# Kernel optimization log

Measured on AMD Instinct MI355X. Metric: run time of the kernel, lower is better.

## Reference

```python
import jax, jax.numpy as jnp
import numpy as np

T, H, W, C, HD, K = 4, 128, 128, 256, 8, 9
F = C // HD


def setup_inputs() -> dict:
    key = jax.random.key(0)
    ks = jax.random.split(key, 6)
    x = jax.random.normal(ks[0], (T, H, W, C), jnp.float32)
    attn = jax.random.uniform(ks[1], (1, HD, T, H, W, K), jnp.float32)
    attn = attn / attn.sum(-1, keepdims=True)  # softmax-normalized neighbor weights
    # integer flow offsets (dt, dh, dw) in [-3, 3], as produced by non-local search
    flows = jax.random.randint(ks[2], (1, HD, T, H, W, K, 3), -3, 4, jnp.int32)
    v_w = jax.random.normal(ks[3], (C, C), jnp.float32) * (C ** -0.5)
    proj_w = jax.random.normal(ks[4], (C, C), jnp.float32) * (C ** -0.5)
    proj_b = jnp.zeros((C,), jnp.float32)
    return dict(x=x, attn=attn, flows=flows, v_w=v_w, proj_w=proj_w, proj_b=proj_b)


def reference(x, attn, flows, v_w, proj_w, proj_b):
    T, H, W, C = x.shape
    HD = attn.shape[1]
    F = C // HD
    # v projection, split heads: [T,H,W,HD,F]
    v = (x @ v_w.T).reshape(T, H, W, HD, F)
    fl = flows[0]  # [HD,T,H,W,K,3] integer offsets (dt, dh, dw)
    tt = jnp.clip(jnp.arange(T)[None, :, None, None, None] + fl[..., 0], 0, T - 1)
    hh = jnp.clip(jnp.arange(H)[None, None, :, None, None] + fl[..., 1], 0, H - 1)
    ww = jnp.clip(jnp.arange(W)[None, None, None, :, None] + fl[..., 2], 0, W - 1)
    hd = jnp.arange(HD)[:, None, None, None, None]
    # flow-guided non-local gather: [HD,T,H,W,K,F]
    gathered = v[tt, hh, ww, hd]
    # attention-weighted sum over K neighbors, merge heads: [T,H,W,C]
    out = jnp.einsum('dthwk,dthwkf->thwdf', attn[0], gathered).reshape(T, H, W, C)
    # output projection
    return out @ proj_w.T + proj_b
```

## Files before the change

### kernel.cpp

```cpp
#include <hip/hip_runtime.h>
#include <hip/hip_bf16.h>

namespace {

constexpr int T = 4, H = 128, W = 128, C = 256, HD = 8, K = 9, F = 32;
constexpr int M = T * H * W;

typedef __attribute__((ext_vector_type(8))) short short8v;
typedef __attribute__((ext_vector_type(4))) float f32x4;

__device__ __forceinline__ unsigned short f2bf(float f) {
  unsigned u = __float_as_uint(f);
  unsigned r = (u + 0x7fffu + ((u >> 16) & 1u)) >> 16;
  return (unsigned short)r;
}

__device__ __forceinline__ float bf2f(unsigned short u) {
  return __uint_as_float(((unsigned)u) << 16);
}

template <int ALAYOUT, bool OUT_F32>
__global__ __launch_bounds__(256) void mfma_gemm(
    const void* __restrict__ Aptr, const float* __restrict__ Bw,
    void* __restrict__ Cptr, const float* __restrict__ bias) {
  __shared__ unsigned short As[128][40];
  __shared__ unsigned short Bs[128][40];
  const int m0 = blockIdx.x * 128;
  const int n0 = blockIdx.y * 128;
  const int t = threadIdx.x;
  const int lane = t & 63;
  const int wid = t >> 6;
  const int wm = wid >> 1, wn = wid & 1;
  const int fr = lane & 15;
  const int kg = lane >> 4;

  f32x4 acc[4][4];
#pragma unroll
  for (int ni = 0; ni < 4; ++ni) {
    float b = 0.f;
    if (OUT_F32) b = bias[n0 + wn * 64 + ni * 16 + fr];
#pragma unroll
    for (int mi = 0; mi < 4; ++mi) {
      acc[mi][ni][0] = b; acc[mi][ni][1] = b;
      acc[mi][ni][2] = b; acc[mi][ni][3] = b;
    }
  }

  for (int k0 = 0; k0 < C; k0 += 32) {
    __syncthreads();
    if (ALAYOUT == 2) {
      const unsigned short* Ab = (const unsigned short*)Aptr;
      const size_t hb = (size_t)(k0 >> 5) * M * 32;
#pragma unroll
      for (int i = 0; i < 2; ++i) {
        const int flat = t + i * 256;
        const int row = flat >> 2, kc = (flat & 3) * 8;
        *(short8v*)&As[row][kc] =
            *(const short8v*)(Ab + hb + (size_t)(m0 + row) * 32 + kc);
      }
    } else {
      const float* Af = (const float*)Aptr;
#pragma unroll
      for (int i = 0; i < 4; ++i) {
        const int flat = t + i * 256;
        const int row = flat >> 3, kc = (flat & 7) * 4;
        const float4 v4 = *(const float4*)(Af + (size_t)(m0 + row) * C + k0 + kc);
        ushort4 o;
        o.x = f2bf(v4.x); o.y = f2bf(v4.y); o.z = f2bf(v4.z); o.w = f2bf(v4.w);
        *(ushort4*)&As[row][kc] = o;
      }
    }
#pragma unroll
    for (int i = 0; i < 4; ++i) {
      const int flat = t + i * 256;
      const int row = flat >> 3, kc = (flat & 7) * 4;
      const float4 v4 = *(const float4*)(Bw + (size_t)(n0 + row) * C + k0 + kc);
      ushort4 o;
      o.x = f2bf(v4.x); o.y = f2bf(v4.y); o.z = f2bf(v4.z); o.w = f2bf(v4.w);
      *(ushort4*)&Bs[row][kc] = o;
    }
    __syncthreads();
    short8v af[4], bfv[4];
#pragma unroll
    for (int mi = 0; mi < 4; ++mi)
      af[mi] = *(const short8v*)&As[wm * 64 + mi * 16 + fr][kg * 8];
#pragma unroll
    for (int ni = 0; ni < 4; ++ni)
      bfv[ni] = *(const short8v*)&Bs[wn * 64 + ni * 16 + fr][kg * 8];
#pragma unroll
    for (int mi = 0; mi < 4; ++mi)
#pragma unroll
      for (int ni = 0; ni < 4; ++ni)
        acc[mi][ni] = __builtin_amdgcn_mfma_f32_16x16x32_bf16(
            af[mi], bfv[ni], acc[mi][ni], 0, 0, 0);
  }

#pragma unroll
  for (int mi = 0; mi < 4; ++mi) {
#pragma unroll
    for (int ni = 0; ni < 4; ++ni) {
      const int gcol = n0 + wn * 64 + ni * 16 + fr;
#pragma unroll
      for (int r = 0; r < 4; ++r) {
        const int grow = m0 + wm * 64 + mi * 16 + kg * 4 + r;
        if (OUT_F32) {
          ((float*)Cptr)[(size_t)grow * C + gcol] = acc[mi][ni][r];
        } else {
          ((unsigned short*)Cptr)[(size_t)grow * C + gcol] = f2bf(acc[mi][ni][r]);
        }
      }
    }
  }
}

struct __attribute__((packed, aligned(4))) I4p { int a, b, c, d; };
struct __attribute__((packed, aligned(4))) I2p { int a, b; };
struct __attribute__((packed, aligned(4))) F4p { float a, b, c, d; };

__global__ __launch_bounds__(256, 4) void gather_lds_kernel(
    const unsigned short* __restrict__ v, const float* __restrict__ attn,
    const int* __restrict__ flows, unsigned short* __restrict__ agg2) {
  __shared__ __align__(16) unsigned short halo[560 * 32];
  const int nb = (blockIdx.x & 7) * 512 + (blockIdx.x >> 3);
  const int head = nb & 7;
  const int tile = nb >> 3;
  const int h0 = (tile >> 5) * 8;
  const int w0 = (tile & 31) * 4;
  const int tid = threadIdx.x;
  const int o = tid >> 1;
  const int fh = tid & 1;
  const int tq = o >> 5;
  const int s = o & 31;
  const int h = h0 + (s >> 2);
  const int w = w0 + (s & 3);
  const int m = (tq << 14) | (h << 7) | w;
  const unsigned short* vhead = v + head * F;

  const int base = ((head << 16) | m) * K;
  const int fb = base * 3;
  const I4p f0 = *(const I4p*)(flows + fb + 0);
  const I4p f1 = *(const I4p*)(flows + fb + 4);
  const I4p f2 = *(const I4p*)(flows + fb + 8);
  const I4p f3 = *(const I4p*)(flows + fb + 12);
  const I4p f4 = *(const I4p*)(flows + fb + 16);
  const I4p f5 = *(const I4p*)(flows + fb + 20);
  const I2p f6 = *(const I2p*)(flows + fb + 24);
  const int f7 = flows[fb + 26];
  const F4p a0 = *(const F4p*)(attn + base + 0);
  const F4p a1 = *(const F4p*)(attn + base + 4);
  const float a2 = attn[base + 8];

  auto piece_src = [&](int pi, int& ldsoff) -> const short8v* {
    const int sliver = pi >> 2, j = pi & 3;
    const int tt = sliver / 140;
    const int rem = sliver - tt * 140;
    const int hh = rem / 10;
    const int ww = rem - hh * 10;
    const int hc = min(max(h0 - 3 + hh, 0), H - 1);
    const int wc = min(max(w0 - 3 + ww, 0), W - 1);
    const int sm = (tt << 14) | (hc << 7) | wc;
    const int jj = (j + (sliver >> 1)) & 3;
    ldsoff = sliver * 32 + jj * 8;
    return (const short8v*)(vhead + (size_t)sm * C + j * 8);
  };
  {
    short8v pc[8]; int lo[8];
#pragma unroll
    for (int e = 0; e < 8; ++e) pc[e] = *piece_src(tid + e * 256, lo[e]);
    short8v pt; int lot = 0;
    if (tid < 192) pt = *piece_src(2048 + tid, lot);
#pragma unroll
    for (int e = 0; e < 8; ++e) *(short8v*)&halo[lo[e]] = pc[e];
    if (tid < 192) *(short8v*)&halo[lot] = pt;
  }

  const int d[27] = {f0.a, f0.b, f0.c, f0.d, f1.a, f1.b, f1.c, f1.d,
                     f2.a, f2.b, f2.c, f2.d, f3.a, f3.b, f3.c, f3.d,
                     f4.a, f4.b, f4.c, f4.d, f5.a, f5.b, f5.c, f5.d,
                     f6.a, f6.b, f7};
  const float aw[9] = {a0.a, a0.b, a0.c, a0.d, a1.a, a1.b, a1.c, a1.d, a2};
  int row[9];
#pragma unroll
  for (int k = 0; k < 9; ++k) {
    const int ts = min(max(tq + d[3 * k + 0], 0), T - 1);
    const int hs = min(max(h + d[3 * k + 1], 0), H - 1) - (h0 - 3);
    const int ws = min(max(w + d[3 * k + 2], 0), W - 1) - (w0 - 3);
    row[k] = (ts * 14 + hs) * 10 + ws;
  }

  __syncthreads();

  float acc[16];
#pragma unroll
  for (int i = 0; i < 16; ++i) acc[i] = 0.f;
#pragma unroll
  for (int k = 0; k < 9; ++k) {
    const int rbase = row[k] * 32;
    const int rot = (row[k] >> 1) & 3;
#pragma unroll
    for (int jl = 0; jl < 2; ++jl) {
      const int j = fh * 2 + jl;
      const short8v p = *(const short8v*)&halo[rbase + (((j + rot) & 3)) * 8];
#pragma unroll
      for (int e = 0; e < 8; ++e)
        acc[jl * 8 + e] += aw[k] * bf2f((unsigned short)p[e]);
    }
  }

  unsigned short* dst = agg2 + ((size_t)head * M + m) * F + fh * 16;
#pragma unroll
  for (int jl = 0; jl < 2; ++jl) {
    short8v ov;
#pragma unroll
    for (int e = 0; e < 8; ++e) ov[e] = (short)f2bf(acc[jl * 8 + e]);
    *(short8v*)(dst + jl * 8) = ov;
  }
}

__global__ __launch_bounds__(256) void agg_proj_kernel(
    const unsigned short* __restrict__ v, const float* __restrict__ attn,
    const int* __restrict__ flows, const float* __restrict__ proj_w,
    const float* __restrict__ proj_b, float* __restrict__ out) {
  __shared__ float Agg[32][C];
  __shared__ float Bs[32][C];
  const int bid = blockIdx.x;
  const int t = bid >> 9;
  const int h0 = ((bid >> 5) & 15) * 8;
  const int w0 = (bid & 31) * 4;
  const int tid = threadIdx.x;

  const int g = tid >> 3;
  const int f4 = (tid & 7) * 4;
#pragma unroll
  for (int r = 0; r < 8; ++r) {
    const int pi = r * 32 + g;
    const int pos = pi >> 3;
    const int head = pi & 7;
    const int h = h0 + (pos >> 2);
    const int w = w0 + (pos & 3);
    const int base = (((head * T + t) * H + h) * W + w) * K;
    const int fbase = base * 3;
    float4 acc = {0.f, 0.f, 0.f, 0.f};
#pragma unroll
    for (int k = 0; k < K; ++k) {
      const int dt = flows[fbase + k * 3 + 0];
      const int dh = flows[fbase + k * 3 + 1];
      const int dw = flows[fbase + k * 3 + 2];
      const float aw = attn[base + k];
      const int tt = min(max(t + dt, 0), T - 1);
      const int hh = min(max(h + dh, 0), H - 1);
      const int ww = min(max(w + dw, 0), W - 1);
      const int mm = (tt * H + hh) * W + ww;
      const ushort4 r4 = *(const ushort4*)(v + (size_t)mm * C + head * F + f4);
      acc.x += aw * bf2f(r4.x);
      acc.y += aw * bf2f(r4.y);
      acc.z += aw * bf2f(r4.z);
      acc.w += aw * bf2f(r4.w);
    }
    *(float4*)&Agg[pos][head * F + f4] = acc;
  }
  __syncthreads();

  const int tx = tid & 31;
  const int ty = tid >> 5;
  float acc2[4][8];
  {
    const float4 b0 = *(const float4*)(proj_b + tx * 8);
    const float4 b1 = *(const float4*)(proj_b + tx * 8 + 4);
#pragma unroll
    for (int i = 0; i < 4; ++i) {
      acc2[i][0] = b0.x; acc2[i][1] = b0.y; acc2[i][2] = b0.z; acc2[i][3] = b0.w;
      acc2[i][4] = b1.x; acc2[i][5] = b1.y; acc2[i][6] = b1.z; acc2[i][7] = b1.w;
    }
  }
  for (int k0 = 0; k0 < C; k0 += 32) {
#pragma unroll
    for (int i = 0; i < 8; ++i) {
      const float4 w4 = *(const float4*)(proj_w + (size_t)tid * C + k0 + i * 4);
      Bs[i * 4 + 0][tid] = w4.x;
      Bs[i * 4 + 1][tid] = w4.y;
      Bs[i * 4 + 2][tid] = w4.z;
      Bs[i * 4 + 3][tid] = w4.w;
    }
    __syncthreads();
#pragma unroll 4
    for (int kk = 0; kk < 32; ++kk) {
      const float4 bb0 = *(const float4*)&Bs[kk][tx * 8];
      const float4 bb1 = *(const float4*)&Bs[kk][tx * 8 + 4];
      float a[4];
#pragma unroll
      for (int i = 0; i < 4; ++i) a[i] = Agg[ty * 4 + i][k0 + kk];
#pragma unroll
      for (int i = 0; i < 4; ++i) {
        acc2[i][0] += a[i] * bb0.x;
        acc2[i][1] += a[i] * bb0.y;
        acc2[i][2] += a[i] * bb0.z;
        acc2[i][3] += a[i] * bb0.w;
        acc2[i][4] += a[i] * bb1.x;
        acc2[i][5] += a[i] * bb1.y;
        acc2[i][6] += a[i] * bb1.z;
        acc2[i][7] += a[i] * bb1.w;
      }
    }
    __syncthreads();
  }
#pragma unroll
  for (int i = 0; i < 4; ++i) {
    const int pos = ty * 4 + i;
    const int h = h0 + (pos >> 2);
    const int w = w0 + (pos & 3);
    const int m = (t * H + h) * W + w;
    float4 o0, o1;
    o0.x = acc2[i][0]; o0.y = acc2[i][1]; o0.z = acc2[i][2]; o0.w = acc2[i][3];
    o1.x = acc2[i][4]; o1.y = acc2[i][5]; o1.z = acc2[i][6]; o1.w = acc2[i][7];
    *(float4*)(out + (size_t)m * C + tx * 8) = o0;
    *(float4*)(out + (size_t)m * C + tx * 8 + 4) = o1;
  }
}

}

extern "C" void kernel_launch(void* const* d_in, const int* in_sizes, int n_in,
                              void* d_out, int out_size, void* d_ws,
                              size_t ws_size, hipStream_t stream) {
  const float* x = (const float*)d_in[0];
  const float* attn = (const float*)d_in[1];
  const int* flows = (const int*)d_in[2];
  const float* v_w = (const float*)d_in[3];
  const float* proj_w = (const float*)d_in[4];
  const float* proj_b = (const float*)d_in[5];
  float* out = (float*)d_out;

  const size_t VBYTES = (size_t)M * C * 2;
  unsigned short* v = (unsigned short*)d_ws;

  dim3 g1(M / 128, C / 128);
  mfma_gemm<0, false><<<g1, 256, 0, stream>>>(x, v_w, v, nullptr);

  if (ws_size >= 2 * VBYTES) {
    unsigned short* agg2 = (unsigned short*)((char*)d_ws + VBYTES);
    gather_lds_kernel<<<4096, 256, 0, stream>>>(v, attn, flows, agg2);
    mfma_gemm<2, true><<<g1, 256, 0, stream>>>(agg2, proj_w, out, proj_b);
  } else {
    const int nblk = T * (H / 8) * (W / 4);
    agg_proj_kernel<<<nblk, 256, 0, stream>>>(v, attn, flows, proj_w, proj_b,
                                              out);
  }
}
```

Baseline: 97.66 us.

## Double-buffer LDS halo tiles and process four w-tiles per block

Each gather block now loops over four consecutive 4-wide w-tiles instead of one. The halo for the next tile and its flow/attn metadata are loaded into registers while the current tile is computed from a second LDS buffer. The goal is to overlap global-memory latency with the LDS gather-accumulate and to amortize block setup. In exchange the kernel needs twice the LDS and more registers, launch bounds drop to 2 blocks per CU, and the grid shrinks to 1024 blocks.

```diff
diff --git a/kernel.cpp b/kernel.cpp
--- a/kernel.cpp
+++ b/kernel.cpp
@@ -117,103 +117,146 @@
 struct __attribute__((packed, aligned(4))) I2p { int a, b; };
 struct __attribute__((packed, aligned(4))) F4p { float a, b, c, d; };
 
-__global__ __launch_bounds__(256, 4) void gather_lds_kernel(
+__global__ __launch_bounds__(256, 2) void gather_lds_kernel(
     const unsigned short* __restrict__ v, const float* __restrict__ attn,
     const int* __restrict__ flows, unsigned short* __restrict__ agg2) {
-  __shared__ __align__(16) unsigned short halo[560 * 32];
-  const int nb = (blockIdx.x & 7) * 512 + (blockIdx.x >> 3);
+  __shared__ __align__(16) unsigned short halo[2][560 * 32];
+  const int nb = (blockIdx.x & 7) * 128 + (blockIdx.x >> 3);
   const int head = nb & 7;
-  const int tile = nb >> 3;
-  const int h0 = (tile >> 5) * 8;
-  const int w0 = (tile & 31) * 4;
+  const int rest = nb >> 3;
+  const int h0 = (rest >> 3) * 8;
+  const int wgp = rest & 7;
+  const int w0base = wgp * 16;
   const int tid = threadIdx.x;
   const int o = tid >> 1;
   const int fh = tid & 1;
   const int tq = o >> 5;
   const int s = o & 31;
-  const int h = h0 + (s >> 2);
-  const int w = w0 + (s & 3);
-  const int m = (tq << 14) | (h << 7) | w;
+  const int hof = s >> 2, wof = s & 3;
+  const int h = h0 + hof;
   const unsigned short* vhead = v + head * F;
 
-  const int base = ((head << 16) | m) * K;
-  const int fb = base * 3;
-  const I4p f0 = *(const I4p*)(flows + fb + 0);
-  const I4p f1 = *(const I4p*)(flows + fb + 4);
-  const I4p f2 = *(const I4p*)(flows + fb + 8);
-  const I4p f3 = *(const I4p*)(flows + fb + 12);
-  const I4p f4 = *(const I4p*)(flows + fb + 16);
-  const I4p f5 = *(const I4p*)(flows + fb + 20);
-  const I2p f6 = *(const I2p*)(flows + fb + 24);
-  const int f7 = flows[fb + 26];
-  const F4p a0 = *(const F4p*)(attn + base + 0);
-  const F4p a1 = *(const F4p*)(attn + base + 4);
-  const float a2 = attn[base + 8];
-
-  auto piece_src = [&](int pi, int& ldsoff) -> const short8v* {
-    const int sliver = pi >> 2, j = pi & 3;
-    const int tt = sliver / 140;
-    const int rem = sliver - tt * 140;
-    const int hh = rem / 10;
-    const int ww = rem - hh * 10;
-    const int hc = min(max(h0 - 3 + hh, 0), H - 1);
-    const int wc = min(max(w0 - 3 + ww, 0), W - 1);
-    const int sm = (tt << 14) | (hc << 7) | wc;
-    const int jj = (j + (sliver >> 1)) & 3;
-    ldsoff = sliver * 32 + jj * 8;
-    return (const short8v*)(vhead + (size_t)sm * C + j * 8);
-  };
-  {
-    short8v pc[8]; int lo[8];
-#pragma unroll
-    for (int e = 0; e < 8; ++e) pc[e] = *piece_src(tid + e * 256, lo[e]);
-    short8v pt; int lot = 0;
-    if (tid < 192) pt = *piece_src(2048 + tid, lot);
-#pragma unroll
-    for (int e = 0; e < 8; ++e) *(short8v*)&halo[lo[e]] = pc[e];
-    if (tid < 192) *(short8v*)&halo[lot] = pt;
-  }
-
-  const int d[27] = {f0.a, f0.b, f0.c, f0.d, f1.a, f1.b, f1.c, f1.d,
-                     f2.a, f2.b, f2.c, f2.d, f3.a, f3.b, f3.c, f3.d,
-                     f4.a, f4.b, f4.c, f4.d, f5.a, f5.b, f5.c, f5.d,
-                     f6.a, f6.b, f7};
-  const float aw[9] = {a0.a, a0.b, a0.c, a0.d, a1.a, a1.b, a1.c, a1.d, a2};
-  int row[9];
-#pragma unroll
-  for (int k = 0; k < 9; ++k) {
-    const int ts = min(max(tq + d[3 * k + 0], 0), T - 1);
-    const int hs = min(max(h + d[3 * k + 1], 0), H - 1) - (h0 - 3);
-    const int ws = min(max(w + d[3 * k + 2], 0), W - 1) - (w0 - 3);
-    row[k] = (ts * 14 + hs) * 10 + ws;
-  }
-
+  short8v pc[8]; int lo[8]; short8v pt; int lot;
+  auto stage_load = [&](int w0t) {
+#pragma unroll
+    for (int e = 0; e < 8; ++e) {
+      const int pi = tid + e * 256;
+      const int sliver = pi >> 2, j = pi & 3;
+      const int tt = sliver / 140;
+      const int rem = sliver - tt * 140;
+      const int hh = rem / 10;
+      const int ww = rem - hh * 10;
+      const int hc = min(max(h0 - 3 + hh, 0), H - 1);
+      const int wc = min(max(w0t - 3 + ww, 0), W - 1);
+      const int sm = (tt << 14) | (hc << 7) | wc;
+      lo[e] = sliver * 32 + ((j + (sliver >> 1)) & 3) * 8;
+      pc[e] = *(const short8v*)(vhead + (size_t)sm * C + j * 8);
+    }
+    lot = -1;
+    if (tid < 192) {
+      const int pi = 2048 + tid;
+      const int sliver = pi >> 2, j = pi & 3;
+      const int tt = sliver / 140;
+      const int rem = sliver - tt * 140;
+      const int hh = rem / 10;
+      const int ww = rem - hh * 10;
+      const int hc = min(max(h0 - 3 + hh, 0), H - 1);
+      const int wc = min(max(w0t - 3 + ww, 0), W - 1);
+      const int sm = (tt << 14) | (hc << 7) | wc;
+      lot = sliver * 32 + ((j + (sliver >> 1)) & 3) * 8;
+      pt = *(const short8v*)(vhead + (size_t)sm * C + j * 8);
+    }
+  };
+  auto stage_write = [&](int buf) {
+    unsigned short* hb = halo[buf];
+#pragma unroll
+    for (int e = 0; e < 8; ++e) *(short8v*)&hb[lo[e]] = pc[e];
+    if (lot >= 0) *(short8v*)&hb[lot] = pt;
+  };
+
+  I4p f0, f1, f2, f3, f4, f5; I2p f6; int f7; F4p a0, a1; float a2;
+  auto meta_load = [&](int w0t) {
+    const int m_ = (tq << 14) | (h << 7) | (w0t + wof);
+    const int base = ((head << 16) | m_) * K;
+    const int fb = base * 3;
+    f0 = *(const I4p*)(flows + fb + 0);
+    f1 = *(const I4p*)(flows + fb + 4);
+    f2 = *(const I4p*)(flows + fb + 8);
+    f3 = *(const I4p*)(flows + fb + 12);
+    f4 = *(const I4p*)(flows + fb + 16);
+    f5 = *(const I4p*)(flows + fb + 20);
+    f6 = *(const I2p*)(flows + fb + 24);
+    f7 = flows[fb + 26];
+    a0 = *(const F4p*)(attn + base + 0);
+    a1 = *(const F4p*)(attn + base + 4);
+    a2 = attn[base + 8];
+  };
+  int rowC[9]; float awC[9];
+  auto meta_decode = [&](int w0t) {
+    const int w_ = w0t + wof;
+    const int d[27] = {f0.a, f0.b, f0.c, f0.d, f1.a, f1.b, f1.c, f1.d,
+                       f2.a, f2.b, f2.c, f2.d, f3.a, f3.b, f3.c, f3.d,
+                       f4.a, f4.b, f4.c, f4.d, f5.a, f5.b, f5.c, f5.d,
+                       f6.a, f6.b, f7};
+    const float aw9[9] = {a0.a, a0.b, a0.c, a0.d, a1.a, a1.b, a1.c, a1.d, a2};
+#pragma unroll
+    for (int k = 0; k < 9; ++k) {
+      const int ts = min(max(tq + d[3 * k + 0], 0), T - 1);
+      const int hs = min(max(h + d[3 * k + 1], 0), H - 1) - (h0 - 3);
+      const int ws = min(max(w_ + d[3 * k + 2], 0), W - 1) - (w0t - 3);
+      rowC[k] = (ts * 14 + hs) * 10 + ws;
+      awC[k] = aw9[k];
+    }
+  };
+
+  auto compute_store = [&](int buf, int w0t) {
+    const unsigned short* hb = halo[buf];
+    float acc[16];
+#pragma unroll
+    for (int i = 0; i < 16; ++i) acc[i] = 0.f;
+#pragma unroll
+    for (int k = 0; k < 9; ++k) {
+      const int rbase = rowC[k] * 32;
+      const int rot = (rowC[k] >> 1) & 3;
+#pragma unroll
+      for (int jl = 0; jl < 2; ++jl) {
+        const int j = fh * 2 + jl;
+        const short8v p = *(const short8v*)&hb[rbase + ((j + rot) & 3) * 8];
+#pragma unroll
+        for (int e = 0; e < 8; ++e)
+          acc[jl * 8 + e] += awC[k] * bf2f((unsigned short)p[e]);
+      }
+    }
+    const int m_ = (tq << 14) | (h << 7) | (w0t + wof);
+    unsigned short* dst = agg2 + ((size_t)head * M + m_) * F + fh * 16;
+#pragma unroll
+    for (int jl = 0; jl < 2; ++jl) {
+      short8v ov;
+#pragma unroll
+      for (int e = 0; e < 8; ++e) ov[e] = (short)f2bf(acc[jl * 8 + e]);
+      *(short8v*)(dst + jl * 8) = ov;
+    }
+  };
+
+  meta_load(w0base);
+  stage_load(w0base);
+  stage_write(0);
+  meta_decode(w0base);
   __syncthreads();
 
-  float acc[16];
-#pragma unroll
-  for (int i = 0; i < 16; ++i) acc[i] = 0.f;
-#pragma unroll
-  for (int k = 0; k < 9; ++k) {
-    const int rbase = row[k] * 32;
-    const int rot = (row[k] >> 1) & 3;
-#pragma unroll
-    for (int jl = 0; jl < 2; ++jl) {
-      const int j = fh * 2 + jl;
-      const short8v p = *(const short8v*)&halo[rbase + (((j + rot) & 3)) * 8];
-#pragma unroll
-      for (int e = 0; e < 8; ++e)
-        acc[jl * 8 + e] += aw[k] * bf2f((unsigned short)p[e]);
-    }
-  }
-
-  unsigned short* dst = agg2 + ((size_t)head * M + m) * F + fh * 16;
-#pragma unroll
-  for (int jl = 0; jl < 2; ++jl) {
-    short8v ov;
-#pragma unroll
-    for (int e = 0; e < 8; ++e) ov[e] = (short)f2bf(acc[jl * 8 + e]);
-    *(short8v*)(dst + jl * 8) = ov;
+#pragma unroll
+  for (int i = 0; i < 4; ++i) {
+    const int cur = i & 1;
+    if (i < 3) {
+      meta_load(w0base + (i + 1) * 4);
+      stage_load(w0base + (i + 1) * 4);
+    }
+    compute_store(cur, w0base + i * 4);
+    if (i < 3) {
+      stage_write(cur ^ 1);
+      meta_decode(w0base + (i + 1) * 4);
+    }
+    __syncthreads();
   }
 }
 
@@ -339,7 +382,7 @@
 
   if (ws_size >= 2 * VBYTES) {
     unsigned short* agg2 = (unsigned short*)((char*)d_ws + VBYTES);
-    gather_lds_kernel<<<4096, 256, 0, stream>>>(v, attn, flows, agg2);
+    gather_lds_kernel<<<1024, 256, 0, stream>>>(v, attn, flows, agg2);
     mfma_gemm<2, true><<<g1, 256, 0, stream>>>(agg2, proj_w, out, proj_b);
   } else {
     const int nblk = T * (H / 8) * (W / 4);
```

Result: slower. 100.6 us (+3.0%).
